# Optimization experiments

Measured on AMD Instinct MI355X. Metric: run time of the kernel, lower is better.

The kernel has to match this reference:

```python
import jax, jax.numpy as jnp
import numpy as np

N_NODES = 100000
N_EDGES = 1600000
N_GRAPHS = 256
IN_DIM, HID = 30, 40

def setup_inputs() -> dict:
    key = jax.random.key(0)
    ks = jax.random.split(key, 12)
    x = jax.random.normal(ks[0], (N_NODES, IN_DIM), dtype=jnp.float32)
    edge_index = jax.random.randint(ks[1], (2, N_EDGES), 0, N_NODES, dtype=jnp.int64)
    batch = jnp.sort(jax.random.randint(ks[2], (N_NODES,), 0, N_GRAPHS, dtype=jnp.int64))
    def glorot(k, shape):
        lim = float(np.sqrt(6.0 / (shape[0] + shape[1])))
        return jax.random.uniform(k, shape, dtype=jnp.float32, minval=-lim, maxval=lim)
    return {
        'x': x, 'edge_index': edge_index, 'batch': batch,
        'W1': glorot(ks[3], (IN_DIM, HID)), 'b1': jnp.zeros((HID,), jnp.float32),
        'W2': glorot(ks[4], (HID, HID)),    'b2': jnp.zeros((HID,), jnp.float32),
        'W3': glorot(ks[5], (HID, HID)),    'b3': jnp.zeros((HID,), jnp.float32),
        'lin_w': glorot(ks[6], (HID, 1)),   'lin_b': jnp.zeros((1,), jnp.float32),
    }

def _gcn_layer(x, src, dst, norm, W, b, n_nodes):
    # x: [N, Fin] -> [N, Fout]; fused gather-matmul-scatter form of GCNConv
    h = x @ W                                   # dense transform first (Fout small)
    msg = h[src] * norm[:, None]                # [E+N, Fout] gather + edge scale
    out = jax.ops.segment_sum(msg, dst, num_segments=n_nodes)
    return out + b

def reference(x, edge_index, batch, W1, b1, W2, b2, W3, b3, lin_w, lin_b):
    n = x.shape[0]
    loops = jnp.arange(n, dtype=edge_index.dtype)
    src = jnp.concatenate([edge_index[0], loops])  # add self loops (GCNConv default)
    dst = jnp.concatenate([edge_index[1], loops])
    deg = jax.ops.segment_sum(jnp.ones_like(dst, dtype=x.dtype), dst, num_segments=n)
    dinv = jax.lax.rsqrt(jnp.maximum(deg, 1.0))    # deg >= 1 thanks to self loops
    norm = dinv[src] * dinv[dst]

    h = jax.nn.relu(_gcn_layer(x, src, dst, norm, W1, b1, n))  # dropout inactive (eval)
    h = jax.nn.relu(_gcn_layer(h, src, dst, norm, W2, b2, n))
    h = jax.nn.relu(_gcn_layer(h, src, dst, norm, W3, b3, n))

    # global_mean_pool over graphs
    g_sum = jax.ops.segment_sum(h, batch, num_segments=N_GRAPHS)
    cnt = jax.ops.segment_sum(jnp.ones((n,), h.dtype), batch, num_segments=N_GRAPHS)
    g = g_sum / jnp.maximum(cnt, 1.0)[:, None]
    return g @ lin_w + lin_b                      # [N_GRAPHS, 1]
```

## Files before the change

### kernel.cpp

```cpp
#include <hip/hip_runtime.h>

#define HID 40
#define RBKT 196
#define BSH 9
#define CAP 12288
#define EPB 4096


__device__ inline unsigned pack2_bf16(float a, float b) {
    unsigned ua = __float_as_uint(a);
    unsigned ub = __float_as_uint(b);
    ua = (ua + 0x7fffu + ((ua >> 16) & 1u)) >> 16;
    ub = (ub + 0x7fffu + ((ub >> 16) & 1u)) & 0xffff0000u;
    return ua | ub;
}

__device__ inline void acc8_bf16(float* acc, uint4 v) {
    acc[0] += __uint_as_float(v.x << 16);
    acc[1] += __uint_as_float(v.x & 0xffff0000u);
    acc[2] += __uint_as_float(v.y << 16);
    acc[3] += __uint_as_float(v.y & 0xffff0000u);
    acc[4] += __uint_as_float(v.z << 16);
    acc[5] += __uint_as_float(v.z & 0xffff0000u);
    acc[6] += __uint_as_float(v.w << 16);
    acc[7] += __uint_as_float(v.w & 0xffff0000u);
}

__global__ void clear_kernel(int* __restrict__ bucket_cnt, float* __restrict__ g_sum, int G) {
    int t = blockIdx.x * blockDim.x + threadIdx.x;
    if (t < RBKT) bucket_cnt[t] = 0;
    if (t < G) g_sum[t] = 0.f;
}


__global__ __launch_bounds__(256) void binA_kernel(
        const int* __restrict__ esrc, const int* __restrict__ edst, int E,
        int* __restrict__ bucket_cnt, int* __restrict__ bucket_data) {
    __shared__ int cnt_l[RBKT];
    __shared__ int base_l[RBKT];
    int t = threadIdx.x;
    for (int b = t; b < RBKT; b += 256) cnt_l[b] = 0;
    __syncthreads();
    int e0 = blockIdx.x * EPB;
    int e1 = min(e0 + EPB, E);
    for (int e = e0 + t; e < e1; e += 256) {
        atomicAdd(&cnt_l[edst[e] >> BSH], 1);
    }
    __syncthreads();
    for (int b = t; b < RBKT; b += 256) {
        int c = cnt_l[b];
        base_l[b] = (c > 0) ? atomicAdd(&bucket_cnt[b], c) : 0;
        cnt_l[b] = 0;
    }
    __syncthreads();
    for (int e = e0 + t; e < e1; e += 256) {
        int d = edst[e];
        int s = esrc[e];
        int b = d >> BSH;
        int off = base_l[b] + atomicAdd(&cnt_l[b], 1);
        if (off < CAP) bucket_data[(size_t)b * CAP + off] = (s << BSH) | (d & 511);
    }
}

__global__ void scan_buckets_kernel(const int* __restrict__ cnt, int* __restrict__ base) {
    __shared__ int s[256];
    int t = threadIdx.x;
    int c = (t < RBKT) ? min(cnt[t], CAP) : 0;
    s[t] = c;
    __syncthreads();
    for (int off = 1; off < 256; off <<= 1) {
        int y = (t >= off) ? s[t - off] : 0;
        __syncthreads();
        s[t] += y;
        __syncthreads();
    }
    if (t < RBKT) base[t] = s[t] - c;
    if (t == RBKT - 1) base[RBKT] = s[t];
}

__global__ __launch_bounds__(256) void buildB_kernel(
        const int* __restrict__ bucket_cnt, const int* __restrict__ bucket_base,
        const int* __restrict__ bucket_data,
        int* __restrict__ rowptr, int* __restrict__ mid, int* __restrict__ csr,
        float* __restrict__ dinv, int n, int half) {
    __shared__ int deg_l[512];
    __shared__ int deg_lo[512];
    __shared__ int off_lo[512];
    __shared__ int off_hi[512];
    __shared__ int ps[256];
    int r = blockIdx.x;
    int t = threadIdx.x;
    int cnt = min(bucket_cnt[r], CAP);
    int base = bucket_base[r];
    int node0 = r << BSH;
    int nr = min(512, n - node0);
    for (int i = t; i < 512; i += 256) { deg_l[i] = 0; deg_lo[i] = 0; }
    __syncthreads();
    const int* data = bucket_data + (size_t)r * CAP;
    for (int e = t; e < cnt; e += 256) {
        int v = data[e];
        atomicAdd(&deg_l[v & 511], 1);
        if ((v >> BSH) < half) atomicAdd(&deg_lo[v & 511], 1);
    }
    __syncthreads();
    int a0 = deg_l[2 * t], a1 = deg_l[2 * t + 1];
    ps[t] = a0 + a1;
    __syncthreads();
    for (int off = 1; off < 256; off <<= 1) {
        int y = (t >= off) ? ps[t - off] : 0;
        __syncthreads();
        ps[t] += y;
        __syncthreads();
    }
    int excl = ps[t] - (a0 + a1);
    off_lo[2 * t] = excl;
    off_lo[2 * t + 1] = excl + a0;
    off_hi[2 * t] = excl + deg_lo[2 * t];
    off_hi[2 * t + 1] = excl + a0 + deg_lo[2 * t + 1];
    __syncthreads();
    for (int i = t; i < nr; i += 256) {
        int rp = base + off_lo[i];
        rowptr[node0 + i] = rp;
        mid[node0 + i] = rp + deg_lo[i];
        dinv[node0 + i] = rsqrtf((float)(deg_l[i] + 1));
    }
    if (r == RBKT - 1 && t == 0) rowptr[n] = base + cnt;
    __syncthreads();
    for (int e = t; e < cnt; e += 256) {
        int v = data[e];
        int s = v >> BSH;
        int d = v & 511;
        int p = (s < half) ? atomicAdd(&off_lo[d], 1) : atomicAdd(&off_hi[d], 1);
        csr[base + p] = s;
    }
}


__global__ __launch_bounds__(256) void scale_bf16_kernel(
        const float* __restrict__ x, const float* __restrict__ dinv,
        unsigned* __restrict__ xs, int n) {
    int t = blockIdx.x * blockDim.x + threadIdx.x;
    int i = t >> 4, p = t & 15;
    if (i >= n) return;
    float a = 0.f, b = 0.f;
    if (p < 15) {
        float d = dinv[i];
        a = x[i * 30 + 2 * p] * d;
        b = x[i * 30 + 2 * p + 1] * d;
    }
    xs[(size_t)i * 16 + p] = pack2_bf16(a, b);
}

template <int INF, int TPN, int OUTF, bool POOL>
__global__ __launch_bounds__(64 * TPN) void fused_layer_kernel(
        const unsigned* __restrict__ xs, const int* __restrict__ rowptr,
        const int* __restrict__ mid, const int* __restrict__ csr,
        const float* __restrict__ dinv,
        const float* __restrict__ W, const float* __restrict__ bias,
        const float* __restrict__ lin_w, const int* __restrict__ batch,
        unsigned* __restrict__ gout, float* __restrict__ g_sum, int n) {
    constexpr int NT  = 64 * TPN;
    constexpr int STR = 8 * TPN + 1;
    constexpr int OPF = OUTF / TPN;
    __shared__ float Ws[INF * OUTF];
    __shared__ float aggs[64 * STR];
    __shared__ float lw[POOL ? OUTF : 1];
    __shared__ float sarr[POOL ? NT : 1];
    const int tid = threadIdx.x;
    for (int t = tid; t < INF * OUTF; t += NT) Ws[t] = W[t];
    if (POOL) {
        for (int t = tid; t < OUTF; t += NT) lw[t] = lin_w[t];
    }
    const int node_l = tid / TPN, q = tid - node_l * TPN;
    const int node = blockIdx.x * 64 + node_l;
    const bool valid = (node < n);
    if (valid) {
        const uint4* tab = reinterpret_cast<const uint4*>(xs);
        float acc[8];
        {
            uint4 v = tab[(size_t)node * TPN + q];
            acc[0] = __uint_as_float(v.x << 16);
            acc[1] = __uint_as_float(v.x & 0xffff0000u);
            acc[2] = __uint_as_float(v.y << 16);
            acc[3] = __uint_as_float(v.y & 0xffff0000u);
            acc[4] = __uint_as_float(v.z << 16);
            acc[5] = __uint_as_float(v.z & 0xffff0000u);
            acc[6] = __uint_as_float(v.w << 16);
            acc[7] = __uint_as_float(v.w & 0xffff0000u);
        }
        int e0 = rowptr[node], m = mid[node], e1 = rowptr[node + 1];
        int e = e0;
        for (; e + 4 <= m; e += 4) {
            int s0 = csr[e], s1 = csr[e + 1], s2 = csr[e + 2], s3 = csr[e + 3];
            uint4 v0 = tab[(size_t)s0 * TPN + q];
            uint4 v1 = tab[(size_t)s1 * TPN + q];
            uint4 v2 = tab[(size_t)s2 * TPN + q];
            uint4 v3 = tab[(size_t)s3 * TPN + q];
            acc8_bf16(acc, v0);
            acc8_bf16(acc, v1);
            acc8_bf16(acc, v2);
            acc8_bf16(acc, v3);
        }
        for (; e < m; e++) {
            acc8_bf16(acc, tab[(size_t)csr[e] * TPN + q]);
        }
        for (; e + 4 <= e1; e += 4) {
            int s0 = csr[e], s1 = csr[e + 1], s2 = csr[e + 2], s3 = csr[e + 3];
            uint4 v0 = tab[(size_t)s0 * TPN + q];
            uint4 v1 = tab[(size_t)s1 * TPN + q];
            uint4 v2 = tab[(size_t)s2 * TPN + q];
            uint4 v3 = tab[(size_t)s3 * TPN + q];
            acc8_bf16(acc, v0);
            acc8_bf16(acc, v1);
            acc8_bf16(acc, v2);
            acc8_bf16(acc, v3);
        }
        for (; e < e1; e++) {
            acc8_bf16(acc, tab[(size_t)csr[e] * TPN + q]);
        }
        float d = dinv[node];
        float* ar = &aggs[node_l * STR + q * 8];
        #pragma unroll
        for (int j = 0; j < 8; j++) ar[j] = acc[j] * d;
    }
    __syncthreads();
    if (POOL) sarr[tid] = 0.f;
    if (valid) {
        const float* arow = &aggs[node_l * STR];
        float acc2[OPF];
        #pragma unroll
        for (int j = 0; j < OPF; j++) acc2[j] = 0.f;
        for (int k = 0; k < INF; k++) {
            float xk = arow[k];
            #pragma unroll
            for (int j = 0; j < OPF; j++) acc2[j] += xk * Ws[k * OUTF + q * OPF + j];
        }
        if (!POOL) {
            float scale = dinv[node];
            unsigned* orow = gout + (size_t)node * (OUTF / 2) + q * (OPF / 2);
            #pragma unroll
            for (int j = 0; j < OPF / 2; j++) {
                int f = q * OPF + 2 * j;
                float v0 = fmaxf(acc2[2 * j] + bias[f], 0.f) * scale;
                float v1 = fmaxf(acc2[2 * j + 1] + bias[f + 1], 0.f) * scale;
                orow[j] = pack2_bf16(v0, v1);
            }
        } else {
            float s = 0.f;
            #pragma unroll
            for (int j = 0; j < OPF; j++) {
                int f = q * OPF + j;
                s += fmaxf(acc2[j] + bias[f], 0.f) * lw[f];
            }
            sarr[tid] = s;
        }
    }
    if (POOL) {
        __syncthreads();
        if (tid < 64) {
            float s = 0.f;
            #pragma unroll
            for (int q2 = 0; q2 < TPN; q2++) s += sarr[tid * TPN + q2];
            int node2 = blockIdx.x * 64 + tid;
            bool v2 = (node2 < n);
            int g = batch[v2 ? node2 : (n - 1)];
            if (!v2) s = 0.f;
            int g0 = __shfl(g, 0, 64);
            if (__all(g == g0)) {
                #pragma unroll
                for (int off = 32; off > 0; off >>= 1) s += __shfl_xor(s, off, 64);
                if (tid == 0) atomicAdd(&g_sum[g0], s);
            } else {
                if (v2) atomicAdd(&g_sum[g], s);
            }
        }
    }
}

__global__ void finalize_kernel(const float* __restrict__ g_sum,
                                const int* __restrict__ batch,
                                const float* __restrict__ lin_b,
                                float* __restrict__ out, int n, int G) {
    int b = blockIdx.x * blockDim.x + threadIdx.x;
    if (b >= G) return;
    int lo = 0, hi = n;
    while (lo < hi) { int m = (lo + hi) >> 1; if (batch[m] < b) lo = m + 1; else hi = m; }
    int lo2 = lo, hi2 = n;
    while (lo2 < hi2) { int m = (lo2 + hi2) >> 1; if (batch[m] < b + 1) lo2 = m + 1; else hi2 = m; }
    int cnt = lo2 - lo;
    out[b] = g_sum[b] / (float)(cnt > 0 ? cnt : 1) + lin_b[0];
}


static inline size_t align_up(size_t v, size_t a) { return (v + a - 1) / a * a; }

extern "C" void kernel_launch(void* const* d_in, const int* in_sizes, int n_in,
                              void* d_out, int out_size, void* d_ws, size_t ws_size,
                              hipStream_t stream) {
    const float* x      = (const float*)d_in[0];
    const int*   esrc   = (const int*)d_in[1];
    const int*   batch  = (const int*)d_in[2];
    const float* W1     = (const float*)d_in[3];
    const float* b1     = (const float*)d_in[4];
    const float* W2     = (const float*)d_in[5];
    const float* b2     = (const float*)d_in[6];
    const float* W3     = (const float*)d_in[7];
    const float* b3     = (const float*)d_in[8];
    const float* lin_w  = (const float*)d_in[9];
    const float* lin_b  = (const float*)d_in[10];
    float* out = (float*)d_out;

    const int n = in_sizes[0] / 30;
    const int E = in_sizes[1] / 2;
    const int G = out_size;
    const int* edst = esrc + E;

    char* w = (char*)d_ws;
    size_t off = 0;
    auto take = [&](size_t bytes) { size_t o = off; off = align_up(off + bytes, 256); return (void*)(w + o); };
    int*      bucket_cnt  = (int*)take((size_t)RBKT * 4);
    int*      bucket_base = (int*)take((size_t)(RBKT + 1) * 4);
    int*      rowptr      = (int*)take((size_t)(n + 1) * 4);
    int*      mid         = (int*)take((size_t)n * 4);
    float*    dinv        = (float*)take((size_t)n * 4);
    int*      csr         = (int*)take((size_t)E * 4);
    float*    g_sum       = (float*)take((size_t)G * 4);
    size_t bd = (size_t)RBKT * CAP * 4;
    size_t x1 = (size_t)n * 16 * 4;
    void* shared_region = take(bd > x1 ? bd : x1);
    int*      bucket_data = (int*)shared_region;
    unsigned* xs1         = (unsigned*)shared_region;
    unsigned* tbA         = (unsigned*)take((size_t)n * 20 * 4);
    unsigned* tbB         = (unsigned*)take((size_t)n * 20 * 4);
    (void)ws_size;

    clear_kernel<<<1, 256, 0, stream>>>(bucket_cnt, g_sum, G);

    binA_kernel<<<(E + EPB - 1) / EPB, 256, 0, stream>>>(esrc, edst, E, bucket_cnt, bucket_data);
    scan_buckets_kernel<<<1, 256, 0, stream>>>(bucket_cnt, bucket_base);
    buildB_kernel<<<RBKT, 256, 0, stream>>>(bucket_cnt, bucket_base, bucket_data,
                                            rowptr, mid, csr, dinv, n, n / 2);

    int nblk = (n + 63) / 64;

    scale_bf16_kernel<<<((size_t)n * 16 + 255) / 256, 256, 0, stream>>>(x, dinv, xs1, n);
    fused_layer_kernel<30, 4, HID, false><<<nblk, 256, 0, stream>>>(
        xs1, rowptr, mid, csr, dinv, W1, b1, nullptr, nullptr, tbA, nullptr, n);
    fused_layer_kernel<HID, 5, HID, false><<<nblk, 320, 0, stream>>>(
        tbA, rowptr, mid, csr, dinv, W2, b2, nullptr, nullptr, tbB, nullptr, n);
    fused_layer_kernel<HID, 5, HID, true><<<nblk, 320, 0, stream>>>(
        tbB, rowptr, mid, csr, dinv, W3, b3, lin_w, batch, nullptr, g_sum, n);

    finalize_kernel<<<1, 256, 0, stream>>>(g_sum, batch, lin_b, out, n, G);
}
```

Measured before the change: 209.6 us.

## Split fused GCN layer into separate gather and dense transform kernels

Each fused gather+matmul layer kernel becomes two kernels. The first is a flat gather/aggregate kernel that writes the aggregated features in bf16 to an intermediate buffer. The second is a transform kernel that loads 64-node tiles into shared memory and applies W, bias, ReLU and pooling. The goal is to decouple the latency-bound gather from the shared-memory matmul, so each part gets better occupancy and no block-wide sync sits between them. The cost is an extra bf16 round trip of the aggregate through global memory, three more kernel launches, and an extra rounding of the aggregate to bf16.

```diff
diff --git a/kernel.cpp b/kernel.cpp
--- a/kernel.cpp
+++ b/kernel.cpp
@@ -151,98 +151,117 @@
     xs[(size_t)i * 16 + p] = pack2_bf16(a, b);
 }
 
-template <int INF, int TPN, int OUTF, bool POOL>
-__global__ __launch_bounds__(64 * TPN) void fused_layer_kernel(
+template <int TPN>
+__global__ __launch_bounds__(256) void gather_bf16_kernel(
         const unsigned* __restrict__ xs, const int* __restrict__ rowptr,
         const int* __restrict__ mid, const int* __restrict__ csr,
-        const float* __restrict__ dinv,
-        const float* __restrict__ W, const float* __restrict__ bias,
+        const float* __restrict__ dinv, unsigned* __restrict__ gout, int n) {
+    int t = blockIdx.x * blockDim.x + threadIdx.x;
+    int i = t / TPN;
+    int q = t - i * TPN;
+    if (i >= n) return;
+    const uint4* tab = reinterpret_cast<const uint4*>(xs);
+    float acc[8];
+    {
+        uint4 v = tab[(size_t)i * TPN + q];
+        acc[0] = __uint_as_float(v.x << 16);
+        acc[1] = __uint_as_float(v.x & 0xffff0000u);
+        acc[2] = __uint_as_float(v.y << 16);
+        acc[3] = __uint_as_float(v.y & 0xffff0000u);
+        acc[4] = __uint_as_float(v.z << 16);
+        acc[5] = __uint_as_float(v.z & 0xffff0000u);
+        acc[6] = __uint_as_float(v.w << 16);
+        acc[7] = __uint_as_float(v.w & 0xffff0000u);
+    }
+    int e0 = rowptr[i], m = mid[i], e1 = rowptr[i + 1];
+    int e = e0;
+    for (; e + 4 <= m; e += 4) {
+        int s0 = csr[e], s1 = csr[e + 1], s2 = csr[e + 2], s3 = csr[e + 3];
+        uint4 v0 = tab[(size_t)s0 * TPN + q];
+        uint4 v1 = tab[(size_t)s1 * TPN + q];
+        uint4 v2 = tab[(size_t)s2 * TPN + q];
+        uint4 v3 = tab[(size_t)s3 * TPN + q];
+        acc8_bf16(acc, v0);
+        acc8_bf16(acc, v1);
+        acc8_bf16(acc, v2);
+        acc8_bf16(acc, v3);
+    }
+    for (; e < m; e++) acc8_bf16(acc, tab[(size_t)csr[e] * TPN + q]);
+    for (; e + 4 <= e1; e += 4) {
+        int s0 = csr[e], s1 = csr[e + 1], s2 = csr[e + 2], s3 = csr[e + 3];
+        uint4 v0 = tab[(size_t)s0 * TPN + q];
+        uint4 v1 = tab[(size_t)s1 * TPN + q];
+        uint4 v2 = tab[(size_t)s2 * TPN + q];
+        uint4 v3 = tab[(size_t)s3 * TPN + q];
+        acc8_bf16(acc, v0);
+        acc8_bf16(acc, v1);
+        acc8_bf16(acc, v2);
+        acc8_bf16(acc, v3);
+    }
+    for (; e < e1; e++) acc8_bf16(acc, tab[(size_t)csr[e] * TPN + q]);
+    float d = dinv[i];
+    uint4 o;
+    o.x = pack2_bf16(acc[0] * d, acc[1] * d);
+    o.y = pack2_bf16(acc[2] * d, acc[3] * d);
+    o.z = pack2_bf16(acc[4] * d, acc[5] * d);
+    o.w = pack2_bf16(acc[6] * d, acc[7] * d);
+    reinterpret_cast<uint4*>(gout)[(size_t)i * TPN + q] = o;
+}
+
+template <int INF, int RU, bool POOL>
+__global__ __launch_bounds__(256) void transform_bf16_kernel(
+        const unsigned* __restrict__ tin, const float* __restrict__ W,
+        const float* __restrict__ bias, const float* __restrict__ dinv,
         const float* __restrict__ lin_w, const int* __restrict__ batch,
-        unsigned* __restrict__ gout, float* __restrict__ g_sum, int n) {
-    constexpr int NT  = 64 * TPN;
-    constexpr int STR = 8 * TPN + 1;
-    constexpr int OPF = OUTF / TPN;
+        unsigned* __restrict__ out, float* __restrict__ g_sum, int n) {
+    constexpr int OUTF = 40;
+    constexpr int OPF  = 10;
     __shared__ float Ws[INF * OUTF];
-    __shared__ float aggs[64 * STR];
+    __shared__ unsigned tile[64 * (RU + 1)];
     __shared__ float lw[POOL ? OUTF : 1];
-    __shared__ float sarr[POOL ? NT : 1];
+    __shared__ float sarr[POOL ? 256 : 1];
     const int tid = threadIdx.x;
-    for (int t = tid; t < INF * OUTF; t += NT) Ws[t] = W[t];
-    if (POOL) {
-        for (int t = tid; t < OUTF; t += NT) lw[t] = lin_w[t];
-    }
-    const int node_l = tid / TPN, q = tid - node_l * TPN;
-    const int node = blockIdx.x * 64 + node_l;
+    for (int t = tid; t < INF * OUTF; t += 256) Ws[t] = W[t];
+    if (POOL && tid < OUTF) lw[tid] = lin_w[tid];
+    const int base = blockIdx.x * 64;
+    const unsigned* g = tin + (size_t)base * RU;
+    const int limit = (n - base) * RU;
+    for (int idx = tid; idx < 64 * RU; idx += 256) {
+        if (idx < limit) {
+            int row = idx / RU, col = idx - row * RU;
+            tile[row * (RU + 1) + col] = g[idx];
+        }
+    }
+    __syncthreads();
+    const int node_l = tid >> 2, q = tid & 3;
+    const int node = base + node_l;
     const bool valid = (node < n);
-    if (valid) {
-        const uint4* tab = reinterpret_cast<const uint4*>(xs);
-        float acc[8];
-        {
-            uint4 v = tab[(size_t)node * TPN + q];
-            acc[0] = __uint_as_float(v.x << 16);
-            acc[1] = __uint_as_float(v.x & 0xffff0000u);
-            acc[2] = __uint_as_float(v.y << 16);
-            acc[3] = __uint_as_float(v.y & 0xffff0000u);
-            acc[4] = __uint_as_float(v.z << 16);
-            acc[5] = __uint_as_float(v.z & 0xffff0000u);
-            acc[6] = __uint_as_float(v.w << 16);
-            acc[7] = __uint_as_float(v.w & 0xffff0000u);
-        }
-        int e0 = rowptr[node], m = mid[node], e1 = rowptr[node + 1];
-        int e = e0;
-        for (; e + 4 <= m; e += 4) {
-            int s0 = csr[e], s1 = csr[e + 1], s2 = csr[e + 2], s3 = csr[e + 3];
-            uint4 v0 = tab[(size_t)s0 * TPN + q];
-            uint4 v1 = tab[(size_t)s1 * TPN + q];
-            uint4 v2 = tab[(size_t)s2 * TPN + q];
-            uint4 v3 = tab[(size_t)s3 * TPN + q];
-            acc8_bf16(acc, v0);
-            acc8_bf16(acc, v1);
-            acc8_bf16(acc, v2);
-            acc8_bf16(acc, v3);
-        }
-        for (; e < m; e++) {
-            acc8_bf16(acc, tab[(size_t)csr[e] * TPN + q]);
-        }
-        for (; e + 4 <= e1; e += 4) {
-            int s0 = csr[e], s1 = csr[e + 1], s2 = csr[e + 2], s3 = csr[e + 3];
-            uint4 v0 = tab[(size_t)s0 * TPN + q];
-            uint4 v1 = tab[(size_t)s1 * TPN + q];
-            uint4 v2 = tab[(size_t)s2 * TPN + q];
-            uint4 v3 = tab[(size_t)s3 * TPN + q];
-            acc8_bf16(acc, v0);
-            acc8_bf16(acc, v1);
-            acc8_bf16(acc, v2);
-            acc8_bf16(acc, v3);
-        }
-        for (; e < e1; e++) {
-            acc8_bf16(acc, tab[(size_t)csr[e] * TPN + q]);
-        }
-        float d = dinv[node];
-        float* ar = &aggs[node_l * STR + q * 8];
-        #pragma unroll
-        for (int j = 0; j < 8; j++) ar[j] = acc[j] * d;
-    }
-    __syncthreads();
     if (POOL) sarr[tid] = 0.f;
     if (valid) {
-        const float* arow = &aggs[node_l * STR];
-        float acc2[OPF];
+        const unsigned* myrow = &tile[node_l * (RU + 1)];
+        float acc[OPF];
         #pragma unroll
-        for (int j = 0; j < OPF; j++) acc2[j] = 0.f;
-        for (int k = 0; k < INF; k++) {
-            float xk = arow[k];
+        for (int j = 0; j < OPF; j++) acc[j] = 0.f;
+        #pragma unroll
+        for (int k2 = 0; k2 < INF / 2; k2++) {
+            unsigned u = myrow[k2];
+            float x0 = __uint_as_float(u << 16);
+            float x1 = __uint_as_float(u & 0xffff0000u);
+            const float* w0 = &Ws[(2 * k2) * OUTF + q * OPF];
+            const float* w1 = &Ws[(2 * k2 + 1) * OUTF + q * OPF];
             #pragma unroll
-            for (int j = 0; j < OPF; j++) acc2[j] += xk * Ws[k * OUTF + q * OPF + j];
+            for (int j = 0; j < OPF; j++) acc[j] += x0 * w0[j];
+            #pragma unroll
+            for (int j = 0; j < OPF; j++) acc[j] += x1 * w1[j];
         }
         if (!POOL) {
-            float scale = dinv[node];
-            unsigned* orow = gout + (size_t)node * (OUTF / 2) + q * (OPF / 2);
+            float d = dinv[node];
+            unsigned* orow = out + (size_t)node * 20 + q * 5;
             #pragma unroll
-            for (int j = 0; j < OPF / 2; j++) {
+            for (int j = 0; j < 5; j++) {
                 int f = q * OPF + 2 * j;
-                float v0 = fmaxf(acc2[2 * j] + bias[f], 0.f) * scale;
-                float v1 = fmaxf(acc2[2 * j + 1] + bias[f + 1], 0.f) * scale;
+                float v0 = fmaxf(acc[2 * j] + bias[f], 0.f) * d;
+                float v1 = fmaxf(acc[2 * j + 1] + bias[f + 1], 0.f) * d;
                 orow[j] = pack2_bf16(v0, v1);
             }
         } else {
@@ -250,7 +269,7 @@
             #pragma unroll
             for (int j = 0; j < OPF; j++) {
                 int f = q * OPF + j;
-                s += fmaxf(acc2[j] + bias[f], 0.f) * lw[f];
+                s += fmaxf(acc[j] + bias[f], 0.f) * lw[f];
             }
             sarr[tid] = s;
         }
@@ -258,20 +277,18 @@
     if (POOL) {
         __syncthreads();
         if (tid < 64) {
-            float s = 0.f;
-            #pragma unroll
-            for (int q2 = 0; q2 < TPN; q2++) s += sarr[tid * TPN + q2];
-            int node2 = blockIdx.x * 64 + tid;
+            float s = sarr[tid * 4] + sarr[tid * 4 + 1] + sarr[tid * 4 + 2] + sarr[tid * 4 + 3];
+            int node2 = base + tid;
             bool v2 = (node2 < n);
-            int g = batch[v2 ? node2 : (n - 1)];
+            int gg = batch[v2 ? node2 : (n - 1)];
             if (!v2) s = 0.f;
-            int g0 = __shfl(g, 0, 64);
-            if (__all(g == g0)) {
+            int g0 = __shfl(gg, 0, 64);
+            if (__all(gg == g0)) {
                 #pragma unroll
                 for (int off = 32; off > 0; off >>= 1) s += __shfl_xor(s, off, 64);
                 if (tid == 0) atomicAdd(&g_sum[g0], s);
             } else {
-                if (v2) atomicAdd(&g_sum[g], s);
+                if (v2) atomicAdd(&g_sum[gg], s);
             }
         }
     }
@@ -330,6 +347,7 @@
     void* shared_region = take(bd > x1 ? bd : x1);
     int*      bucket_data = (int*)shared_region;
     unsigned* xs1         = (unsigned*)shared_region;
+    unsigned* agg         = (unsigned*)take((size_t)n * 20 * 4);
     unsigned* tbA         = (unsigned*)take((size_t)n * 20 * 4);
     unsigned* tbB         = (unsigned*)take((size_t)n * 20 * 4);
     (void)ws_size;
@@ -341,15 +359,21 @@
     buildB_kernel<<<RBKT, 256, 0, stream>>>(bucket_cnt, bucket_base, bucket_data,
                                             rowptr, mid, csr, dinv, n, n / 2);
 
-    int nblk = (n + 63) / 64;
+    int nblk64 = (n + 63) / 64;
 
     scale_bf16_kernel<<<((size_t)n * 16 + 255) / 256, 256, 0, stream>>>(x, dinv, xs1, n);
-    fused_layer_kernel<30, 4, HID, false><<<nblk, 256, 0, stream>>>(
-        xs1, rowptr, mid, csr, dinv, W1, b1, nullptr, nullptr, tbA, nullptr, n);
-    fused_layer_kernel<HID, 5, HID, false><<<nblk, 320, 0, stream>>>(
-        tbA, rowptr, mid, csr, dinv, W2, b2, nullptr, nullptr, tbB, nullptr, n);
-    fused_layer_kernel<HID, 5, HID, true><<<nblk, 320, 0, stream>>>(
-        tbB, rowptr, mid, csr, dinv, W3, b3, lin_w, batch, nullptr, g_sum, n);
+    gather_bf16_kernel<4><<<((size_t)n * 4 + 255) / 256, 256, 0, stream>>>(
+        xs1, rowptr, mid, csr, dinv, agg, n);
+    transform_bf16_kernel<30, 16, false><<<nblk64, 256, 0, stream>>>(
+        agg, W1, b1, dinv, nullptr, nullptr, tbA, nullptr, n);
+    gather_bf16_kernel<5><<<((size_t)n * 5 + 255) / 256, 256, 0, stream>>>(
+        tbA, rowptr, mid, csr, dinv, agg, n);
+    transform_bf16_kernel<40, 20, false><<<nblk64, 256, 0, stream>>>(
+        agg, W2, b2, dinv, nullptr, nullptr, tbB, nullptr, n);
+    gather_bf16_kernel<5><<<((size_t)n * 5 + 255) / 256, 256, 0, stream>>>(
+        tbB, rowptr, mid, csr, dinv, agg, n);
+    transform_bf16_kernel<40, 20, true><<<nblk64, 256, 0, stream>>>(
+        agg, W3, b3, dinv, lin_w, batch, nullptr, g_sum, n);
 
     finalize_kernel<<<1, 256, 0, stream>>>(g_sum, batch, lin_b, out, n, G);
 }
```

Measured after the change: 216.6 us. +3.4%, slower.
